# Optimization experiments

Measured on AMD Instinct MI355X. Metric: run time of the kernel, lower is better.

## Reference

```python
import jax, jax.numpy as jnp
import numpy as np

CHANNELS = 256
N_HEADS = 8
WS = 8
HEAD_DIM = CHANNELS // N_HEADS
SCALE = HEAD_DIM ** -0.5
EPS = 1e-5


def setup_inputs() -> dict:
    key = jax.random.key(0)
    ks = jax.random.split(key, 7)
    C = CHANNELS
    B, T, H, W = 2, 4, 64, 64
    x = jax.random.normal(ks[0], (B * T, C, H, W), dtype=jnp.float32)
    s = 1.0 / np.sqrt(C)
    w_qkv = jax.random.uniform(ks[1], (3 * C, C), jnp.float32, -s, s)
    b_qkv = jax.random.uniform(ks[2], (3 * C,), jnp.float32, -s, s)
    w_proj = jax.random.uniform(ks[3], (C, C), jnp.float32, -s, s)
    b_proj = jax.random.uniform(ks[4], (C,), jnp.float32, -s, s)
    gamma = jnp.ones((C,), jnp.float32)
    beta = jnp.zeros((C,), jnp.float32)
    return {"x": x, "w_qkv": w_qkv, "b_qkv": b_qkv, "w_proj": w_proj,
            "b_proj": b_proj, "gamma": gamma, "beta": beta, "T": T}


def _forward(x, w_qkv, b_qkv, w_proj, b_proj, gamma, beta, T):
    BT, C, H, W = x.shape
    B = BT // T
    ws = WS
    pH = (ws - H % ws) % ws
    pW = (ws - W % ws) % ws
    if pH > 0 or pW > 0:
        x_p = jnp.pad(x, ((0, 0), (0, 0), (0, pH), (0, pW)))
    else:
        x_p = x
    Hp, Wp = H + pH, W + pW
    nH, nW = Hp // ws, Wp // ws
    # partition: (B,T,C,nH,ws,nW,ws) -> (B,nH,nW,T,ws,ws,C) -> (B*nH*nW, T*ws*ws, C)
    xw = x_p.reshape(B, T, C, nH, ws, nW, ws)
    xw = jnp.transpose(xw, (0, 3, 5, 1, 4, 6, 2))
    L = T * ws * ws
    xw = xw.reshape(B * nH * nW, L, C)
    # LayerNorm over channels
    mu = jnp.mean(xw, axis=-1, keepdims=True)
    var = jnp.mean(jnp.square(xw - mu), axis=-1, keepdims=True)
    xn = (xw - mu) * jax.lax.rsqrt(var + EPS) * gamma + beta
    # QKV projection
    qkv = xn @ w_qkv.T + b_qkv  # (NW, L, 3C)
    qkv = qkv.reshape(xw.shape[0], L, 3, N_HEADS, HEAD_DIM)
    q, k, v = qkv[:, :, 0], qkv[:, :, 1], qkv[:, :, 2]  # (NW, L, h, d)
    scores = jnp.einsum('nlhd,nmhd->nhlm', q, k) * SCALE
    attn = jax.nn.softmax(scores, axis=-1)
    out = jnp.einsum('nhlm,nmhd->nlhd', attn, v).reshape(xw.shape[0], L, C)
    out = out @ w_proj.T + b_proj
    out = xw + out
    # unpartition
    out = out.reshape(B, nH, nW, T, ws, ws, C)
    out = jnp.transpose(out, (0, 3, 6, 1, 4, 2, 5)).reshape(B * T, C, Hp, Wp)
    if pH > 0 or pW > 0:
        out = out[:, :, :H, :W]
    return out


def reference(x, w_qkv, b_qkv, w_proj, b_proj, gamma, beta, T):
    return _forward(x, w_qkv, b_qkv, w_proj, b_proj, gamma, beta, T)
```

## Files before the change

kernel.cpp:

```cpp
#include <hip/hip_runtime.h>
#include <hip/hip_bf16.h>

typedef __hip_bfloat16 bf16;
typedef __attribute__((ext_vector_type(8))) short short8;
typedef __attribute__((ext_vector_type(4))) short sh4;
typedef __attribute__((ext_vector_type(4))) float f32x4;

#define SCALE_F 0.17677669529663687f
#define LOG2E_F 1.4426950408889634f
#define EPS_F 1e-5f
#define NW_CHUNK 32
#define ROWS_CHUNK (NW_CHUNK * 256)

#define OW_QKV  0
#define OW_PROJ 196608
#define OB_QKV  262144
#define OB_PROJ 262912
#define NWB     263168

__device__ __forceinline__ float b2f(bf16 v) { return __bfloat162float(v); }
__device__ __forceinline__ bf16 f2b(float v) { return __float2bfloat16(v); }
__device__ __forceinline__ short f2bs(float v) { bf16 h = f2b(v); return *(short*)&h; }
__device__ __forceinline__ float bs2f(short s) { bf16 h = *(bf16*)&s; return __bfloat162float(h); }

#if __has_builtin(__builtin_amdgcn_exp2f)
__device__ __forceinline__ float fexp2(float x) { return __builtin_amdgcn_exp2f(x); }
#else
__device__ __forceinline__ float fexp2(float x) { return exp2f(x); }
#endif
#if __has_builtin(__builtin_amdgcn_rcpf)
__device__ __forceinline__ float frcp(float x) { return __builtin_amdgcn_rcpf(x); }
#else
__device__ __forceinline__ float frcp(float x) { return 1.0f / x; }
#endif

__device__ __forceinline__ float ldin(const void* p, size_t i, int mode) {
  if (mode) return ((const float*)p)[i];
  return b2f(((const bf16*)p)[i]);
}
__device__ __forceinline__ void stout(void* p, size_t i, int mode, float v) {
  if (mode) ((float*)p)[i] = v;
  else      ((bf16*)p)[i] = f2b(v);
}
__device__ __forceinline__ float4 ldin4(const void* p, size_t i, int mode) {
  if (mode) return *(const float4*)((const float*)p + i);
  const sh4 s = *(const sh4*)((const short*)p + i);
  return make_float4(bs2f(s[0]), bs2f(s[1]), bs2f(s[2]), bs2f(s[3]));
}
__device__ __forceinline__ void stout4(void* p, size_t i, int mode, float4 v) {
  if (mode) { *(float4*)((float*)p + i) = v; }
  else {
    sh4 s; s[0] = f2bs(v.x); s[1] = f2bs(v.y); s[2] = f2bs(v.z); s[3] = f2bs(v.w);
    *(sh4*)((short*)p + i) = s;
  }
}

__device__ __forceinline__ int probe_mode(const float* xf, int tid) {
  __shared__ int s_cnt;
  if (tid == 0) s_cnt = 0;
  __syncthreads();
  int bad = 0;
#pragma unroll
  for (int i = 0; i < 4; ++i) {
    const float v = xf[tid * 4 + i];
    if (!(fabsf(v) < 1e20f)) bad++;
  }
  if (bad) atomicAdd(&s_cnt, bad);
  __syncthreads();
  return (s_cnt < 8) ? 1 : 0;
}

__device__ __forceinline__ void gld16(void* lds, const void* g) {
  __builtin_amdgcn_global_load_lds(
      (const __attribute__((address_space(1))) unsigned int*)g,
      (__attribute__((address_space(3))) unsigned int*)lds, 16, 0, 0);
}

__global__ __launch_bounds__(256) void k_ln(const void* __restrict__ x,
                                            const void* __restrict__ gamma,
                                            const void* __restrict__ beta,
                                            bf16* __restrict__ xn,
                                            const void* __restrict__ w1,
                                            const void* __restrict__ w2,
                                            const void* __restrict__ b1,
                                            const void* __restrict__ b2,
                                            short* __restrict__ wbuf) {
  const int tid = threadIdx.x;
  const int mode = probe_mode((const float*)x, tid);

  {
    const int base = (blockIdx.x * 256 + tid) * 2;
#pragma unroll
    for (int e = 0; e < 2; ++e) {
      const int i = base + e;
      float v;
      if (i < OW_PROJ)      v = ldin(w1, i, mode);
      else if (i < OB_QKV)  v = ldin(w2, i - OW_PROJ, mode);
      else if (i < OB_PROJ) v = ldin(b1, i - OB_QKV, mode);
      else                  v = ldin(b2, i - OB_PROJ, mode);
      wbuf[i] = f2bs(v);
    }
    if (blockIdx.x == 0) {
#pragma unroll
      for (int e = 0; e < 4; ++e) {
        const int i = 262144 + tid * 4 + e;
        float v;
        if (i < OB_PROJ) v = ldin(b1, i - OB_QKV, mode);
        else             v = ldin(b2, i - OB_PROJ, mode);
        wbuf[i] = f2bs(v);
      }
    }
  }

  const int bt = blockIdx.x >> 6;
  const int h  = blockIdx.x & 63;
  const int cl = tid >> 4;
  const int wi = tid & 15;

  __shared__ short sX[256][68];
  __shared__ float sred[16][65];
  __shared__ float sqred[16][65];
  __shared__ float smu[64], srs[64];
  __shared__ float sGm[256], sBt[256];

  sGm[tid] = ldin(gamma, tid, mode);
  sBt[tid] = ldin(beta, tid, mode);

  const size_t gbase = (size_t)bt * 1048576 + (size_t)h * 64 + wi * 4;
  float s4[4] = {0.f, 0.f, 0.f, 0.f}, q4[4] = {0.f, 0.f, 0.f, 0.f};
  for (int c0 = 0; c0 < 256; c0 += 16) {
    const int c = c0 + cl;
    const float4 v = ldin4(x, gbase + (size_t)c * 4096, mode);
    s4[0] += v.x; q4[0] += v.x * v.x;
    s4[1] += v.y; q4[1] += v.y * v.y;
    s4[2] += v.z; q4[2] += v.z * v.z;
    s4[3] += v.w; q4[3] += v.w * v.w;
    sh4 b;
    b[0] = f2bs(v.x); b[1] = f2bs(v.y); b[2] = f2bs(v.z); b[3] = f2bs(v.w);
    *(sh4*)&sX[c][wi * 4] = b;
  }
#pragma unroll
  for (int k = 0; k < 4; ++k) {
    sred[cl][wi * 4 + k] = s4[k];
    sqred[cl][wi * 4 + k] = q4[k];
  }
  __syncthreads();
  if (tid < 64) {
    float a = 0.f, q = 0.f;
#pragma unroll
    for (int g = 0; g < 16; ++g) { a += sred[g][tid]; q += sqred[g][tid]; }
    const float mu = a * (1.0f / 256.0f);
    const float var = fmaxf(q * (1.0f / 256.0f) - mu * mu, 0.0f);
    smu[tid] = mu; srs[tid] = rsqrtf(var + EPS_F);
  }
  __syncthreads();

  {
    const int wtok = tid >> 2;
    const int iw2 = wtok >> 3, s2 = wtok & 7;
    const int cg = (tid & 3) * 64;
    const float mu2 = smu[wtok], rs2 = srs[wtok];
    const int n2 = (bt >> 2) * 64 + (h >> 3) * 8 + iw2;
    const int l2 = (bt & 3) * 64 + (h & 7) * 8 + s2;
    short* xns = (short*)xn;
    const size_t addr = ((size_t)n2 * 256 + l2) * 256 + cg;
#pragma unroll
    for (int k = 0; k < 64; k += 4) {
      sh4 o;
#pragma unroll
      for (int e = 0; e < 4; ++e) {
        const int c = cg + k + e;
        const float v = bs2f(sX[c][wtok]);
        o[e] = f2bs((v - mu2) * rs2 * sGm[c] + sBt[c]);
      }
      *(sh4*)&xns[addr + k] = o;
    }
  }
}

__global__ __launch_bounds__(256) void k_qkv(const bf16* __restrict__ A,
                                             const short* __restrict__ wb,
                                             bf16* __restrict__ out,
                                             int row_base) {
  __shared__ short smem[2 * 128 * 64];
  short* sA = smem;
  short* sB = smem + 128 * 64;
  const int row0 = blockIdx.x * 128;
  const int col0 = blockIdx.y * 128;
  const int tid = threadIdx.x;
  const int wid = tid >> 6, lane = tid & 63;
  const int wy = wid >> 1, wx = wid & 1;
  const int l15 = lane & 15, quad = lane >> 4;
  const short* Ab = (const short*)A;

  const int lr = lane >> 3;
  const int swc = (lane & 7) ^ lr;

  f32x4 acc[4][4];
#pragma unroll
  for (int i = 0; i < 4; ++i)
#pragma unroll
    for (int j = 0; j < 4; ++j) acc[i][j] = (f32x4){0.f, 0.f, 0.f, 0.f};

  for (int k0 = 0; k0 < 256; k0 += 64) {
    if (k0) __syncthreads();
#pragma unroll
    for (int it = 0; it < 4; ++it) {
      const int rbase = wid * 32 + it * 8;
      gld16(sA + rbase * 64,
            Ab + (size_t)(row_base + row0 + rbase + lr) * 256 + k0 + swc * 8);
      gld16(sB + rbase * 64,
            wb + (size_t)(col0 + rbase + lr) * 256 + k0 + swc * 8);
    }
    asm volatile("s_waitcnt vmcnt(0)" ::: "memory");
    __syncthreads();
#pragma unroll
    for (int kk = 0; kk < 64; kk += 32) {
      const int ck = kk >> 3;
      short8 af[4], bfv[4];
#pragma unroll
      for (int i = 0; i < 4; ++i) {
        const int ar = wy * 64 + i * 16 + l15;
        af[i] = *(const short8*)(sA + ar * 64 + (((quad + ck) ^ (ar & 7)) * 8));
      }
#pragma unroll
      for (int j = 0; j < 4; ++j) {
        const int br = wx * 64 + j * 16 + l15;
        bfv[j] = *(const short8*)(sB + br * 64 + (((quad + ck) ^ (br & 7)) * 8));
      }
#pragma unroll
      for (int i = 0; i < 4; ++i)
#pragma unroll
        for (int j = 0; j < 4; ++j)
          acc[i][j] = __builtin_amdgcn_mfma_f32_16x16x32_bf16(af[i], bfv[j], acc[i][j], 0, 0, 0);
    }
  }

  __syncthreads();
  short* slab = smem + wid * (64 * 64);
#pragma unroll
  for (int j = 0; j < 4; ++j) {
    const int col = col0 + wx * 64 + j * 16 + l15;
    const float bj = bs2f(wb[OB_QKV + col]);
#pragma unroll
    for (int i = 0; i < 4; ++i)
#pragma unroll
      for (int r = 0; r < 4; ++r)
        slab[(i * 16 + quad * 4 + r) * 64 + j * 16 + l15] = f2bs(acc[i][j][r] + bj);
  }
  {
    const int srow = lane >> 3;
    const int scol = (lane & 7) * 8;
    short* og = (short*)out;
#pragma unroll
    for (int it = 0; it < 8; ++it) {
      const int rloc = it * 8 + srow;
      short8 v = *(const short8*)&slab[rloc * 64 + scol];
      *(short8*)&og[(size_t)(row0 + wy * 64 + rloc) * 768 + col0 + wx * 64 + scol] = v;
    }
  }
}

__global__ __launch_bounds__(256) void k_attn(const bf16* __restrict__ qkv,
                                              bf16* __restrict__ aout,
                                              int n_base, int nw_mask, int nw_shift) {
  const int n_loc = blockIdx.x & nw_mask, hh = blockIdx.x >> nw_shift;
  const int n_glob = n_base + n_loc;
  __shared__ short sK[256][32];
  __shared__ short sVt[32][256];
  __shared__ short sP[4][16][64];
  const int tid = threadIdx.x;
  const int wid = tid >> 6, lane = tid & 63;
  const int l15 = lane & 15, quad = lane >> 4;
  const int l7 = l15 & 7;
  const short* qg = (const short*)qkv;
  const size_t base = (size_t)n_loc * 256 * 768 + hh * 32;

#pragma unroll
  for (int it = 0; it < 4; ++it) {
    const int rbase = wid * 64 + it * 16;
    gld16(&sK[rbase][0],
          qg + base + (size_t)(rbase + (lane >> 2)) * 768 + 256 + (lane & 3) * 8);
  }
  for (int c = tid; c < 1024; c += 256) {
    const int m = c >> 2, d0 = (c & 3) * 8;
    short8 vv = *(const short8*)(qg + base + (size_t)m * 768 + 512 + d0);
#pragma unroll
    for (int j = 0; j < 8; ++j)
      sVt[d0 + j][(((m >> 3) ^ j) << 3) | (m & 7)] = vv[j];
  }
  asm volatile("s_waitcnt vmcnt(0)" ::: "memory");
  __syncthreads();

  const int R0 = wid * 64;
  const float esc = SCALE_F * LOG2E_F;

  for (int lt = 0; lt < 4; ++lt) {
    const int lrow = R0 + lt * 16;
    const short8 qf = *(const short8*)(qg + base + (size_t)(lrow + l15) * 768 + quad * 8);

    f32x4 sacc[16];
    __builtin_amdgcn_s_setprio(1);
#pragma unroll
    for (int t = 0; t < 16; ++t) {
      sacc[t] = (f32x4){0.f, 0.f, 0.f, 0.f};
      const short8 kf = *(const short8*)&sK[t * 16 + l15][quad * 8];
      sacc[t] = __builtin_amdgcn_mfma_f32_16x16x32_bf16(kf, qf, sacc[t], 0, 0, 0);
    }
    __builtin_amdgcn_s_setprio(0);

    float sum = 0.f;
    f32x4 oacc[2] = {(f32x4){0.f, 0.f, 0.f, 0.f}, (f32x4){0.f, 0.f, 0.f, 0.f}};

#pragma unroll
    for (int ph = 0; ph < 4; ++ph) {
#pragma unroll
      for (int tp = 0; tp < 4; ++tp) {
        const int t = ph * 4 + tp;
        const float p0 = fexp2(sacc[t][0] * esc);
        const float p1 = fexp2(sacc[t][1] * esc);
        const float p2 = fexp2(sacc[t][2] * esc);
        const float p3 = fexp2(sacc[t][3] * esc);
        sum += (p0 + p1) + (p2 + p3);
        sh4 w;
        w[0] = f2bs(p0); w[1] = f2bs(p1); w[2] = f2bs(p2); w[3] = f2bs(p3);
        const int chunk = tp * 2 + (quad >> 1);
        *(sh4*)&sP[wid][l15][((chunk ^ l7) << 3) | ((quad & 1) * 4)] = w;
      }
      __builtin_amdgcn_s_setprio(1);
#pragma unroll
      for (int kk = 0; kk < 2; ++kk) {
        const int pphys = (kk * 4 + quad) ^ l7;
        const short8 pf = *(const short8*)&sP[wid][l15][pphys * 8];
#pragma unroll
        for (int dt = 0; dt < 2; ++dt) {
          const int vrow = dt * 16 + l15;
          const int cch = ph * 8 + kk * 4 + quad;
          const short8 vf = *(const short8*)&sVt[vrow][((cch ^ (vrow & 7)) * 8)];
          oacc[dt] = __builtin_amdgcn_mfma_f32_16x16x32_bf16(vf, pf, oacc[dt], 0, 0, 0);
        }
      }
      __builtin_amdgcn_s_setprio(0);
    }

    sum += __shfl_xor(sum, 16, 64);
    sum += __shfl_xor(sum, 32, 64);
    const float inv = frcp(sum);

    {
      short* og = (short*)aout;
      const size_t obase =
          ((size_t)n_glob * 256 + lrow + l15) * 256 + hh * 32 + quad * 4;
#pragma unroll
      for (int dt = 0; dt < 2; ++dt) {
        sh4 w;
#pragma unroll
        for (int r = 0; r < 4; ++r) w[r] = f2bs(oacc[dt][r] * inv);
        *(sh4*)&og[obase + dt * 16] = w;
      }
    }
  }
}

__global__ __launch_bounds__(256) void k_proj_g(const bf16* __restrict__ A,
                                                const short* __restrict__ wb,
                                                bf16* __restrict__ out) {
  __shared__ short smem[2 * 128 * 64];
  short* sA = smem;
  short* sB = smem + 128 * 64;
  const int row0 = blockIdx.x * 128;
  const int col0 = blockIdx.y * 128;
  const int tid = threadIdx.x;
  const int wid = tid >> 6, lane = tid & 63;
  const int wy = wid >> 1, wx = wid & 1;
  const int l15 = lane & 15, quad = lane >> 4;
  const short* Ab = (const short*)A;

  const int lr = lane >> 3;
  const int swc = (lane & 7) ^ lr;

  f32x4 acc[4][4];
#pragma unroll
  for (int i = 0; i < 4; ++i)
#pragma unroll
    for (int j = 0; j < 4; ++j) acc[i][j] = (f32x4){0.f, 0.f, 0.f, 0.f};

  for (int k0 = 0; k0 < 256; k0 += 64) {
    if (k0) __syncthreads();
#pragma unroll
    for (int it = 0; it < 4; ++it) {
      const int rbase = wid * 32 + it * 8;
      gld16(sA + rbase * 64,
            Ab + (size_t)(row0 + rbase + lr) * 256 + k0 + swc * 8);
      gld16(sB + rbase * 64,
            wb + OW_PROJ + (size_t)(col0 + rbase + lr) * 256 + k0 + swc * 8);
    }
    asm volatile("s_waitcnt vmcnt(0)" ::: "memory");
    __syncthreads();
#pragma unroll
    for (int kk = 0; kk < 64; kk += 32) {
      const int ck = kk >> 3;
      short8 af[4], bfv[4];
#pragma unroll
      for (int i = 0; i < 4; ++i) {
        const int ar = wy * 64 + i * 16 + l15;
        af[i] = *(const short8*)(sA + ar * 64 + (((quad + ck) ^ (ar & 7)) * 8));
      }
#pragma unroll
      for (int j = 0; j < 4; ++j) {
        const int br = wx * 64 + j * 16 + l15;
        bfv[j] = *(const short8*)(sB + br * 64 + (((quad + ck) ^ (br & 7)) * 8));
      }
#pragma unroll
      for (int i = 0; i < 4; ++i)
#pragma unroll
        for (int j = 0; j < 4; ++j)
          acc[i][j] = __builtin_amdgcn_mfma_f32_16x16x32_bf16(af[i], bfv[j], acc[i][j], 0, 0, 0);
    }
  }

  __syncthreads();
  short* slab = smem + wid * (64 * 64);
#pragma unroll
  for (int j = 0; j < 4; ++j) {
    const int col = col0 + wx * 64 + j * 16 + l15;
    const float bj = bs2f(wb[OB_PROJ + col]);
#pragma unroll
    for (int i = 0; i < 4; ++i)
#pragma unroll
      for (int r = 0; r < 4; ++r)
        slab[(i * 16 + quad * 4 + r) * 64 + j * 16 + l15] = f2bs(acc[i][j][r] + bj);
  }
  {
    const int srow = lane >> 3;
    const int scol = (lane & 7) * 8;
    short* og = (short*)out;
#pragma unroll
    for (int it = 0; it < 8; ++it) {
      const int rloc = it * 8 + srow;
      short8 v = *(const short8*)&slab[rloc * 64 + scol];
      *(short8*)&og[(size_t)(row0 + wy * 64 + rloc) * 256 + col0 + wx * 64 + scol] = v;
    }
  }
}

__global__ __launch_bounds__(256) void k_add(const bf16* __restrict__ tmp,
                                             const void* __restrict__ x,
                                             void* __restrict__ out) {
  const int tid = threadIdx.x;
  const int mode = probe_mode((const float*)x, tid);
  const int bt = blockIdx.x >> 6;
  const int h  = blockIdx.x & 63;

  __shared__ short sT2[256][68];

  const int n_b = (bt >> 2) * 64 + (h >> 3) * 8;
  const int l0  = (bt & 3) * 64 + (h & 7) * 8;
  const short* tg = (const short*)tmp;

#pragma unroll
  for (int i = 0; i < 8; ++i) {
    const int id = i * 256 + tid;
    const int w = id >> 5, c8 = (id & 31) * 8;
    const int row = (n_b + (w >> 3)) * 256 + l0 + (w & 7);
    const short8 v = *(const short8*)(tg + (size_t)row * 256 + c8);
    const int wg = ((w >> 2) ^ ((id & 31) & 15)) * 4 + (w & 3);
#pragma unroll
    for (int j = 0; j < 8; ++j) sT2[c8 + j][wg] = v[j];
  }
  __syncthreads();

  const int cl = tid >> 4;
  const int wi = tid & 15;
  const size_t gb = (size_t)bt * 1048576 + (size_t)h * 64 + wi * 4;
  for (int c0 = 0; c0 < 256; c0 += 16) {
    const int c = c0 + cl;
    const int k15 = (c >> 3) & 15;
    const sh4 pv = *(const sh4*)&sT2[c][((wi ^ k15) & 15) * 4];
    const size_t gaddr = gb + (size_t)c * 4096;
    const float4 xv = ldin4(x, gaddr, mode);
    float4 o;
    o.x = xv.x + bs2f(pv[0]);
    o.y = xv.y + bs2f(pv[1]);
    o.z = xv.z + bs2f(pv[2]);
    o.w = xv.w + bs2f(pv[3]);
    stout4(out, gaddr, mode, o);
  }
}

__global__ __launch_bounds__(256) void k_proj(const bf16* __restrict__ A,
                                              const short* __restrict__ wb,
                                              const void* __restrict__ x,
                                              void* __restrict__ out) {
  const int tid = threadIdx.x;
  const int mode = probe_mode((const float*)x, tid);
  __shared__ short smem[2 * 128 * 64];
  __shared__ float sT[4][16][17];
  short* sA = smem;
  short* sB = smem + 128 * 64;
  const int row0 = blockIdx.x * 128;
  const int col0 = blockIdx.y * 128;
  const int wid = tid >> 6, lane = tid & 63;
  const int wy = wid >> 1, wx = wid & 1;
  const int l15 = lane & 15, quad = lane >> 4;
  const short* Ab = (const short*)A;

  const int lr = lane >> 3;
  const int swc = (lane & 7) ^ lr;

  f32x4 acc[4][4];
#pragma unroll
  for (int i = 0; i < 4; ++i)
#pragma unroll
    for (int j = 0; j < 4; ++j) acc[i][j] = (f32x4){0.f, 0.f, 0.f, 0.f};

  for (int k0 = 0; k0 < 256; k0 += 64) {
    if (k0) __syncthreads();
#pragma unroll
    for (int it = 0; it < 4; ++it) {
      const int rbase = wid * 32 + it * 8;
      gld16(sA + rbase * 64,
            Ab + (size_t)(row0 + rbase + lr) * 256 + k0 + swc * 8);
      gld16(sB + rbase * 64,
            wb + OW_PROJ + (size_t)(col0 + rbase + lr) * 256 + k0 + swc * 8);
    }
    asm volatile("s_waitcnt vmcnt(0)" ::: "memory");
    __syncthreads();
#pragma unroll
    for (int kk = 0; kk < 64; kk += 32) {
      const int ck = kk >> 3;
      short8 af[4], bfv[4];
#pragma unroll
      for (int i = 0; i < 4; ++i) {
        const int ar = wy * 64 + i * 16 + l15;
        af[i] = *(const short8*)(sA + ar * 64 + (((quad + ck) ^ (ar & 7)) * 8));
      }
#pragma unroll
      for (int j = 0; j < 4; ++j) {
        const int br = wx * 64 + j * 16 + l15;
        bfv[j] = *(const short8*)(sB + br * 64 + (((quad + ck) ^ (br & 7)) * 8));
      }
#pragma unroll
      for (int i = 0; i < 4; ++i)
#pragma unroll
        for (int j = 0; j < 4; ++j)
          acc[i][j] = __builtin_amdgcn_mfma_f32_16x16x32_bf16(af[i], bfv[j], acc[i][j], 0, 0, 0);
    }
  }

#pragma unroll
  for (int i = 0; i < 4; ++i) {
#pragma unroll
    for (int j = 0; j < 4; ++j) {
#pragma unroll
      for (int r = 0; r < 4; ++r)
        sT[wid][quad * 4 + r][l15] = acc[i][j][r];
      asm volatile("s_waitcnt lgkmcnt(0)" ::: "memory");
#pragma unroll
      for (int r2 = 0; r2 < 4; ++r2) {
        const float v = sT[wid][l15][quad * 4 + r2];
        const int row = row0 + wy * 64 + i * 16 + l15;
        const int c   = col0 + wx * 64 + j * 16 + quad * 4 + r2;
        const int n = row >> 8, l = row & 255;
        const int b = n >> 6, ih = (n >> 3) & 7, iw = n & 7;
        const int tt = l >> 6, rr = (l >> 3) & 7, ss = l & 7;
        const int btl = b * 4 + tt;
        const size_t gaddr = (size_t)btl * 1048576 + (size_t)c * 4096 +
                             (ih * 8 + rr) * 64 + iw * 8 + ss;
        const float o = v + bs2f(wb[OB_PROJ + c]) + ldin(x, gaddr, mode);
        stout(out, gaddr, mode, o);
      }
      asm volatile("s_waitcnt lgkmcnt(0)" ::: "memory");
    }
  }
}

extern "C" void kernel_launch(void* const* d_in, const int* in_sizes, int n_in,
                              void* d_out, int out_size, void* d_ws, size_t ws_size,
                              hipStream_t stream) {
  (void)in_sizes; (void)n_in; (void)out_size;
  const void* x      = d_in[0];
  const void* w_qkv  = d_in[1];
  const void* b_qkv  = d_in[2];
  const void* w_proj = d_in[3];
  const void* b_proj = d_in[4];
  const void* gamma  = d_in[5];
  const void* beta   = d_in[6];

  char* ws = (char*)d_ws;
  short* wbuf  = (short*)(ws + 1024);
  bf16* xnbuf  = (bf16*)(ws + 1024 + 526336);
  bf16* qkvb   = (bf16*)(ws + 1024 + 526336 + 16777216);

  const size_t need_full = 1024 + 526336 + 16777216 + (size_t)32768 * 768 * 2;

  hipLaunchKernelGGL(k_ln, dim3(512), dim3(256), 0, stream, x, gamma, beta, xnbuf,
                     w_qkv, w_proj, b_qkv, b_proj, wbuf);

  if (ws_size >= need_full) {
    hipLaunchKernelGGL(k_qkv, dim3(256, 6), dim3(256), 0, stream,
                       xnbuf, wbuf, qkvb, 0);
    hipLaunchKernelGGL(k_attn, dim3(1024), dim3(256), 0, stream,
                       qkvb, xnbuf, 0, 127, 7);
    bf16* tmpb = qkvb;
    hipLaunchKernelGGL(k_proj_g, dim3(256, 2), dim3(256), 0, stream,
                       xnbuf, wbuf, tmpb);
    hipLaunchKernelGGL(k_add, dim3(512), dim3(256), 0, stream,
                       tmpb, x, d_out);
  } else {
    for (int c = 0; c < 4; ++c) {
      hipLaunchKernelGGL(k_qkv, dim3(64, 6), dim3(256), 0, stream,
                         xnbuf, wbuf, qkvb, c * ROWS_CHUNK);
      hipLaunchKernelGGL(k_attn, dim3(NW_CHUNK * 8), dim3(256), 0, stream,
                         qkvb, xnbuf, c * NW_CHUNK, NW_CHUNK - 1, 5);
    }
    hipLaunchKernelGGL(k_proj, dim3(256, 2), dim3(256), 0, stream,
                       xnbuf, wbuf, x, d_out);
  }
}
```

Baseline: 170.7 us.

## Fuse output projection with residual add and unpartition into one kernel

Merges the projection GEMM and the residual-add/unpartition kernel. Each block now computes a 64-row by 256-column output tile, with rows chosen to match one (bt, h) image row, so the result can be transposed through LDS and added to x directly. This removes the bf16 round trip of the projection output through global memory and one kernel launch. In exchange, each block reloads the full 256x256 projection weight, uses a narrower row tile with more LDS per block, and can keep fewer blocks resident.

```diff
diff --git a/kernel.cpp b/kernel.cpp
--- a/kernel.cpp
+++ b/kernel.cpp
@@ -362,129 +362,95 @@
   }
 }
 
-__global__ __launch_bounds__(256) void k_proj_g(const bf16* __restrict__ A,
-                                                const short* __restrict__ wb,
-                                                bf16* __restrict__ out) {
-  __shared__ short smem[2 * 128 * 64];
+__global__ __launch_bounds__(256) void k_projadd(const bf16* __restrict__ A,
+                                                 const short* __restrict__ wb,
+                                                 const void* __restrict__ x,
+                                                 void* __restrict__ out) {
+  const int tid = threadIdx.x;
+  const int mode = probe_mode((const float*)x, tid);
+  __shared__ short smem[64 * 64 + 256 * 64];
   short* sA = smem;
-  short* sB = smem + 128 * 64;
-  const int row0 = blockIdx.x * 128;
-  const int col0 = blockIdx.y * 128;
-  const int tid = threadIdx.x;
+  short* sB = smem + 64 * 64;
+  const int bt = blockIdx.x >> 6;
+  const int h  = blockIdx.x & 63;
   const int wid = tid >> 6, lane = tid & 63;
-  const int wy = wid >> 1, wx = wid & 1;
   const int l15 = lane & 15, quad = lane >> 4;
   const short* Ab = (const short*)A;
 
+  const int n_b = (bt >> 2) * 64 + (h >> 3) * 8;
+  const int l0  = (bt & 3) * 64 + (h & 7) * 8;
+
   const int lr = lane >> 3;
   const int swc = (lane & 7) ^ lr;
 
-  f32x4 acc[4][4];
-#pragma unroll
-  for (int i = 0; i < 4; ++i)
-#pragma unroll
-    for (int j = 0; j < 4; ++j) acc[i][j] = (f32x4){0.f, 0.f, 0.f, 0.f};
+  f32x4 acc[16];
+#pragma unroll
+  for (int j = 0; j < 16; ++j) acc[j] = (f32x4){0.f, 0.f, 0.f, 0.f};
 
   for (int k0 = 0; k0 < 256; k0 += 64) {
     if (k0) __syncthreads();
 #pragma unroll
-    for (int it = 0; it < 4; ++it) {
-      const int rbase = wid * 32 + it * 8;
-      gld16(sA + rbase * 64,
-            Ab + (size_t)(row0 + rbase + lr) * 256 + k0 + swc * 8);
-      gld16(sB + rbase * 64,
-            wb + OW_PROJ + (size_t)(col0 + rbase + lr) * 256 + k0 + swc * 8);
+    for (int it = 0; it < 2; ++it) {
+      const int rt = wid * 16 + it * 8;
+      const int grow = (n_b + (rt >> 3)) * 256 + l0 + lr;
+      gld16(sA + rt * 64, Ab + (size_t)grow * 256 + k0 + swc * 8);
+    }
+#pragma unroll
+    for (int it = 0; it < 8; ++it) {
+      const int rb = wid * 64 + it * 8;
+      gld16(sB + rb * 64,
+            wb + OW_PROJ + (size_t)(rb + lr) * 256 + k0 + swc * 8);
     }
     asm volatile("s_waitcnt vmcnt(0)" ::: "memory");
     __syncthreads();
 #pragma unroll
     for (int kk = 0; kk < 64; kk += 32) {
       const int ck = kk >> 3;
-      short8 af[4], bfv[4];
-#pragma unroll
-      for (int i = 0; i < 4; ++i) {
-        const int ar = wy * 64 + i * 16 + l15;
-        af[i] = *(const short8*)(sA + ar * 64 + (((quad + ck) ^ (ar & 7)) * 8));
-      }
-#pragma unroll
-      for (int j = 0; j < 4; ++j) {
-        const int br = wx * 64 + j * 16 + l15;
-        bfv[j] = *(const short8*)(sB + br * 64 + (((quad + ck) ^ (br & 7)) * 8));
-      }
-#pragma unroll
-      for (int i = 0; i < 4; ++i)
-#pragma unroll
-        for (int j = 0; j < 4; ++j)
-          acc[i][j] = __builtin_amdgcn_mfma_f32_16x16x32_bf16(af[i], bfv[j], acc[i][j], 0, 0, 0);
-    }
-  }
-
-  __syncthreads();
-  short* slab = smem + wid * (64 * 64);
-#pragma unroll
-  for (int j = 0; j < 4; ++j) {
-    const int col = col0 + wx * 64 + j * 16 + l15;
-    const float bj = bs2f(wb[OB_PROJ + col]);
-#pragma unroll
-    for (int i = 0; i < 4; ++i)
-#pragma unroll
-      for (int r = 0; r < 4; ++r)
-        slab[(i * 16 + quad * 4 + r) * 64 + j * 16 + l15] = f2bs(acc[i][j][r] + bj);
-  }
+      const int ar = wid * 16 + l15;
+      const short8 af = *(const short8*)(sA + ar * 64 + (((quad + ck) ^ (ar & 7)) * 8));
+#pragma unroll
+      for (int j = 0; j < 16; ++j) {
+        const int br = j * 16 + l15;
+        const short8 bfv = *(const short8*)(sB + br * 64 + (((quad + ck) ^ (br & 7)) * 8));
+        acc[j] = __builtin_amdgcn_mfma_f32_16x16x32_bf16(af, bfv, acc[j], 0, 0, 0);
+      }
+    }
+  }
+
+  __syncthreads();
+  short* sT2 = smem;
   {
-    const int srow = lane >> 3;
-    const int scol = (lane & 7) * 8;
-    short* og = (short*)out;
-#pragma unroll
-    for (int it = 0; it < 8; ++it) {
-      const int rloc = it * 8 + srow;
-      short8 v = *(const short8*)&slab[rloc * 64 + scol];
-      *(short8*)&og[(size_t)(row0 + wy * 64 + rloc) * 256 + col0 + wx * 64 + scol] = v;
-    }
-  }
-}
-
-__global__ __launch_bounds__(256) void k_add(const bf16* __restrict__ tmp,
-                                             const void* __restrict__ x,
-                                             void* __restrict__ out) {
-  const int tid = threadIdx.x;
-  const int mode = probe_mode((const float*)x, tid);
-  const int bt = blockIdx.x >> 6;
-  const int h  = blockIdx.x & 63;
-
-  __shared__ short sT2[256][68];
-
-  const int n_b = (bt >> 2) * 64 + (h >> 3) * 8;
-  const int l0  = (bt & 3) * 64 + (h & 7) * 8;
-  const short* tg = (const short*)tmp;
-
-#pragma unroll
-  for (int i = 0; i < 8; ++i) {
-    const int id = i * 256 + tid;
-    const int w = id >> 5, c8 = (id & 31) * 8;
-    const int row = (n_b + (w >> 3)) * 256 + l0 + (w & 7);
-    const short8 v = *(const short8*)(tg + (size_t)row * 256 + c8);
-    const int wg = ((w >> 2) ^ ((id & 31) & 15)) * 4 + (w & 3);
-#pragma unroll
-    for (int j = 0; j < 8; ++j) sT2[c8 + j][wg] = v[j];
-  }
-  __syncthreads();
-
-  const int cl = tid >> 4;
-  const int wi = tid & 15;
-  const size_t gb = (size_t)bt * 1048576 + (size_t)h * 64 + wi * 4;
-  for (int c0 = 0; c0 < 256; c0 += 16) {
-    const int c = c0 + cl;
-    const int k15 = (c >> 3) & 15;
-    const sh4 pv = *(const sh4*)&sT2[c][((wi ^ k15) & 15) * 4];
-    const size_t gaddr = gb + (size_t)c * 4096;
-    const float4 xv = ldin4(x, gaddr, mode);
-    float4 o;
-    o.x = xv.x + bs2f(pv[0]);
-    o.y = xv.y + bs2f(pv[1]);
-    o.z = xv.z + bs2f(pv[2]);
-    o.w = xv.w + bs2f(pv[3]);
-    stout4(out, gaddr, mode, o);
+    const int wq = wid * 4 + quad;
+#pragma unroll
+    for (int j = 0; j < 16; ++j) {
+      const int c = j * 16 + l15;
+      const float bj = bs2f(wb[OB_PROJ + c]);
+      const int col = ((wq ^ ((c >> 3) & 15)) & 15) * 4;
+      sh4 o;
+#pragma unroll
+      for (int r = 0; r < 4; ++r) o[r] = f2bs(acc[j][r] + bj);
+      *(sh4*)&sT2[c * 68 + col] = o;
+    }
+  }
+  __syncthreads();
+
+  {
+    const int cl = tid >> 4;
+    const int wi = tid & 15;
+    const size_t gb = (size_t)bt * 1048576 + (size_t)h * 64 + wi * 4;
+    for (int c0 = 0; c0 < 256; c0 += 16) {
+      const int c = c0 + cl;
+      const int k15 = (c >> 3) & 15;
+      const sh4 pv = *(const sh4*)&sT2[c * 68 + ((wi ^ k15) & 15) * 4];
+      const size_t gaddr = gb + (size_t)c * 4096;
+      const float4 xv = ldin4(x, gaddr, mode);
+      float4 o;
+      o.x = xv.x + bs2f(pv[0]);
+      o.y = xv.y + bs2f(pv[1]);
+      o.z = xv.z + bs2f(pv[2]);
+      o.w = xv.w + bs2f(pv[3]);
+      stout4(out, gaddr, mode, o);
+    }
   }
 }
 
@@ -602,11 +568,8 @@
                        xnbuf, wbuf, qkvb, 0);
     hipLaunchKernelGGL(k_attn, dim3(1024), dim3(256), 0, stream,
                        qkvb, xnbuf, 0, 127, 7);
-    bf16* tmpb = qkvb;
-    hipLaunchKernelGGL(k_proj_g, dim3(256, 2), dim3(256), 0, stream,
-                       xnbuf, wbuf, tmpb);
-    hipLaunchKernelGGL(k_add, dim3(512), dim3(256), 0, stream,
-                       tmpb, x, d_out);
+    hipLaunchKernelGGL(k_projadd, dim3(512), dim3(256), 0, stream,
+                       xnbuf, wbuf, x, d_out);
   } else {
     for (int c = 0; c < 4; ++c) {
       hipLaunchKernelGGL(k_qkv, dim3(64, 6), dim3(256), 0, stream,
```

Result: faster. 164.8 us (-3.5%).
